# Kernel tuning notes

Hardware: AMD Instinct MI355X
Metric: run time of the kernel (lower is better)

Reference implementation:

```python
import jax, jax.numpy as jnp
import numpy as np

N = 4096
DEG = 16.0
KC = 64  # max closed-neighborhood size supported (deg~16 graph => safe)


def setup_inputs() -> dict:
    key = jax.random.key(0)
    ks = jax.random.split(key, 6)
    u = jax.random.uniform(ks[0], (N, N))
    upper = jnp.triu((u < (DEG / N)).astype(jnp.float32), k=1)
    adj = upper + upper.T  # symmetric 0/1, zero diagonal
    d = 64
    return {
        'adj': adj,
        'e_w': jax.random.normal(ks[1], (15, d), dtype=jnp.float32) * 0.25,
        'e_b': jnp.zeros((d,), jnp.float32),
        'w1': jax.random.normal(ks[2], (3, d, d), dtype=jnp.float32) * 0.125,
        'b1': jnp.zeros((3, d), jnp.float32),
        'w2': jax.random.normal(ks[3], (3, d, d), dtype=jnp.float32) * 0.125,
        'b2': jnp.zeros((3, d), jnp.float32),
        'eps': jnp.zeros((3,), jnp.float32),
    }


def cr_feat(adj):
    n = adj.shape[0]
    m = adj + jnp.eye(n, dtype=adj.dtype)  # closed-neighborhood indicator rows [N,N]
    k = m.sum(1)                            # |S_v|
    D = m @ adj                             # D[v,u] = degree of u inside S_v (A symmetric)
    E = 0.5 * jnp.sum(m * D, axis=1)        # edges inside S_v
    W = jnp.sum(m * D * (D - 1.0) * 0.5, axis=1)  # wedges inside S_v
    vals, idx = jax.lax.top_k(m, KC)        # members of S_v (padded)
    valid = (vals > 0.5).astype(adj.dtype)
    sub = adj[idx[:, :, None], idx[:, None, :]]        # [N,KC,KC] induced subgraph
    sub = sub * valid[:, :, None] * valid[:, None, :]
    T = jnp.einsum('vij,vjk,vki->v', sub, sub, sub) / 6.0  # triangles inside S_v
    f3 = T
    f2 = W - 3.0 * T
    f1 = E * (k - 2.0) - 2.0 * f2 - 3.0 * f3
    tot = k * (k - 1.0) * (k - 2.0) / 6.0   # C(k,3) = total triples
    f0 = tot - f1 - f2 - f3
    f = jnp.stack([f0, f1, f2, f3], axis=1)
    f = jnp.where((k >= 3.0)[:, None], f, 0.0)  # original skips |nb|<3
    return f / (jnp.sum(f, axis=1, keepdims=True) + 1e-10)


def ww_feat(adj):
    a2 = adj @ adj
    a4 = a2 @ a2                             # matrix_power(adj, 4)
    vals, _ = jax.lax.top_k(a4, 8)           # per-row sort desc, top 8
    return vals


def degree_feat(adj):
    d = adj.sum(1)
    diag_a2 = jnp.einsum('vu,uv->v', adj, adj)  # diag(A@A)
    return jnp.stack([d, d ** 2, diag_a2], axis=1)


def _forward(adj, e_w, e_b, w1, b1, w2, b2, eps):
    feats = jnp.concatenate([cr_feat(adj), ww_feat(adj), degree_feat(adj)], axis=1)  # [N,15]
    x = feats @ e_w + e_b
    for i in range(3):
        h = (1.0 + eps[i]) * x + adj @ x
        x = jax.nn.relu(h @ w1[i] + b1[i]) @ w2[i] + b2[i]
    return x.sum(0)


def reference(adj, e_w, e_b, w1, b1, w2, b2, eps):
    return _forward(adj, e_w, e_b, w1, b1, w2, b2, eps)
```

## Files before the change

kernel.cpp:

```cpp
#include <hip/hip_runtime.h>
#include <hip/hip_bf16.h>
#include <stdint.h>

#define NN 4096


__global__ __launch_bounds__(256) void scan_k(const float* __restrict__ adj,
                                              int* __restrict__ nbr,
                                              int* __restrict__ deg,
                                              unsigned long long* __restrict__ abits,
                                              float* __restrict__ feats) {
    __shared__ int nlist[4][64];
    int tid = threadIdx.x;
    int wv = tid >> 6, ln = tid & 63;
    int v = blockIdx.x * 4 + wv;
    size_t rb = (size_t)v * NN;
    int total = 0;
    unsigned long long w0 = 0;
    const float4* row4 = (const float4*)(adj + rb);
    for (int base = 0; base < NN; base += 256) {
        float4 f = row4[(base >> 2) + ln];
        int q4 = (base >> 8) << 2;
        #pragma unroll
        for (int j = 0; j < 4; j++) {
            float vj = (j == 0) ? f.x : (j == 1) ? f.y : (j == 2) ? f.z : f.w;
            unsigned long long m = __ballot(vj > 0.5f);
            if (vj > 0.5f) {
                int pos = total + __popcll(m & ((1ull << ln) - 1ull));
                if (pos < 64) nlist[wv][pos] = base + 4 * ln + j;
            }
            if (ln == q4 + j) w0 = m;
            total += __popcll(m);
        }
    }
    abits[(size_t)v * 64 + ln] = w0;
    int degL = min(total, 64);
    if (ln < degL) nbr[v * 64 + ln] = nlist[wv][ln];
    if (ln == 0) {
        deg[v] = total;
        float degf = (float)total;
        feats[v * 16 + 12] = degf;
        feats[v * 16 + 13] = degf * degf;
        feats[v * 16 + 14] = degf;
    }
}

__global__ __launch_bounds__(256) void cra2_k(const unsigned long long* __restrict__ abits,
                                              const int* __restrict__ nbr,
                                              const int* __restrict__ deg,
                                              unsigned int* __restrict__ a3n,
                                              unsigned int* __restrict__ side,
                                              unsigned int* __restrict__ scnt,
                                              float* __restrict__ feats) {
    __shared__ __align__(64) unsigned int smem[NN + 132 + 640];
    int tid = threadIdx.x;
    int bid = blockIdx.x;
    int wv = tid >> 6, ln = tid & 63;

    if (bid < NN) {
        unsigned int* acc   = smem;
        int* us             = (int*)(smem + NN);
        int* dus            = (int*)(smem + NN + 64);
        unsigned int* wsumS = smem + NN + 128;
        unsigned int* srcL  = smem + NN + 132;
        int v = bid;
        uint4 z = {0u, 0u, 0u, 0u};
        #pragma unroll
        for (int i = 0; i < 4; i++) ((uint4*)acc)[tid + 256 * i] = z;
        int dv = min(deg[v], 64);
        if (tid < dv) {
            int u = nbr[v * 64 + tid];
            us[tid] = u;
            dus[tid] = min(deg[u], 64);
        }
        __syncthreads();
        for (int p = tid; p < dv * 64; p += 256) {
            int i = p >> 6, wi = p & 63;
            if (wi < dus[i]) atomicAdd(&acc[nbr[us[i] * 64 + wi]], 1u);
        }
        __syncthreads();
        unsigned int myw[16];
        int local = 0;
        #pragma unroll
        for (int m = 0; m < 16; m++) {
            unsigned int a = acc[tid + 256 * m];
            myw[m] = a;
            local += (a != 0u);
        }
        int incl = local;
        #pragma unroll
        for (int off = 1; off < 64; off <<= 1) {
            int n = __shfl_up(incl, off, 64);
            if (ln >= off) incl += n;
        }
        if (ln == 63) wsumS[wv] = (unsigned int)incl;
        __syncthreads();
        unsigned int wpre = 0, nsrc = 0;
        #pragma unroll
        for (int q = 0; q < 4; q++) {
            unsigned int s = wsumS[q];
            if (q < wv) wpre += s;
            nsrc += s;
        }
        unsigned int pos = wpre + (unsigned int)(incl - local);
        #pragma unroll
        for (int m = 0; m < 16; m++) {
            unsigned int a = myw[m];
            if (a) {
                unsigned int col = (unsigned int)tid + 256u * m;
                unsigned int dgu = (unsigned int)min(deg[col], 64);
                if (pos < 640u) srcL[pos] = (a << 19) | (dgu << 12) | col;
                pos++;
            }
        }
        if (nsrc > 640u) nsrc = 640u;
        __syncthreads();
        #pragma unroll
        for (int i = 0; i < 4; i++) ((uint4*)acc)[tid + 256 * i] = z;
        __syncthreads();
        int lim64 = (((int)nsrc + 1) >> 1) << 6;
        for (int q = tid; q < lim64; q += 256) {
            int s = ((q >> 6) << 1) | ((q >> 5) & 1);
            int j = q & 31;
            if (s < (int)nsrc) {
                unsigned int e = srcL[s];
                int dgu = (int)((e >> 12) & 0x7Fu);
                unsigned int w = e >> 19;
                const int* nru = nbr + (e & 0xFFFu) * 64;
                if (j < dgu) atomicAdd(&acc[nru[j]], w);
                if (j == 31) {
                    for (int jj = 32; jj < dgu; jj++) atomicAdd(&acc[nru[jj]], w);
                }
            }
        }
        __syncthreads();
        unsigned int wAn = 0, wBn = 0, ovm = 0;
        #pragma unroll
        for (int i2 = 0; i2 < 8; i2++) {
            unsigned int a = acc[16 * tid + i2];
            wAn |= min(a, 15u) << (4 * i2);
            ovm |= (a > 15u ? 1u : 0u) << i2;
        }
        #pragma unroll
        for (int i2 = 0; i2 < 8; i2++) {
            unsigned int a = acc[16 * tid + 8 + i2];
            wBn |= min(a, 15u) << (4 * i2);
            ovm |= (a > 15u ? 1u : 0u) << (8 + i2);
        }
        {
            uint2 nw; nw.x = wAn; nw.y = wBn;
            ((uint2*)(a3n + (size_t)v * 512))[tid] = nw;
        }
        int lov = __popc(ovm);
        int inc2 = lov;
        #pragma unroll
        for (int off = 1; off < 64; off <<= 1) {
            int n = __shfl_up(inc2, off, 64);
            if (ln >= off) inc2 += n;
        }
        if (ln == 63) wsumS[wv] = (unsigned int)inc2;
        __syncthreads();
        unsigned int wpre2 = 0, totS = 0;
        #pragma unroll
        for (int q = 0; q < 4; q++) {
            unsigned int s = wsumS[q];
            if (q < wv) wpre2 += s;
            totS += s;
        }
        unsigned int pos2 = wpre2 + (unsigned int)(inc2 - lov);
        unsigned int* sideR = side + (size_t)v * 192;
        while (ovm) {
            int i2 = __ffs(ovm) - 1;
            ovm &= ovm - 1;
            unsigned int col = (unsigned int)(16 * tid + i2);
            unsigned int a = acc[col];
            if (pos2 < 192u) sideR[pos2] = ((a - 15u) << 16) | col;
            pos2++;
        }
        if (tid == 0) scnt[v] = min(totS, 192u);
    } else {
        unsigned long long* rows = (unsigned long long*)smem;
        int* mems = (int*)(smem + 1024);
        int v = (bid - NN) * 4 + wv;

        int dv = deg[v];
        int degL = min(dv, 64);
        int c = min(dv + 1, 64);

        int nl = (ln < degL) ? nbr[v * 64 + ln] : 0;
        int isless = (ln < degL && nl < v) ? 1 : 0;
        int pos = isless;
        #pragma unroll
        for (int off = 32; off; off >>= 1) pos += __shfl_xor(pos, off, 64);

        int mem = 0;
        if (ln < c) {
            if (ln < pos)       mem = nl;
            else if (ln == pos) mem = v;
            else                mem = nbr[v * 64 + ln - 1];
        }
        mems[wv * 64 + ln] = mem;
        __syncthreads();

        unsigned long long mask = 0ull;
        {
            const unsigned long long* rowb = abits + (size_t)mem * 64;
            for (int j = 0; j < c; j++) {
                int mj = mems[wv * 64 + j];
                unsigned long long w = rowb[((mj >> 8) << 2) | (mj & 3)];
                mask |= ((w >> ((mj >> 2) & 63)) & 1ull) << j;
            }
        }
        if (ln >= c) mask = 0ull;
        rows[wv * 64 + ln] = mask;
        __syncthreads();

        int tpart = 0;
        float epart = 0.f, wpart = 0.f;
        if (ln < c) {
            unsigned long long mm = mask;
            while (mm) {
                int j = __ffsll(mm) - 1;
                mm &= mm - 1;
                tpart += __popcll(mask & rows[wv * 64 + j]);
            }
            if (ln != pos) {
                int cn = __popcll(rows[wv * 64 + pos] & mask);
                float D2 = (float)cn + 1.0f;
                epart = D2;
                wpart = D2 * (D2 - 1.0f) * 0.5f;
            }
        }
        float es = epart, wsum2 = wpart;
        int ts = tpart;
        #pragma unroll
        for (int off = 32; off; off >>= 1) {
            es += __shfl_xor(es, off, 64);
            wsum2 += __shfl_xor(wsum2, off, 64);
            ts += __shfl_xor(ts, off, 64);
        }

        if (ln == 0) {
            float degf = (float)dv;
            float k = degf + 1.0f;
            float E = 0.5f * (es + degf);
            float W = wsum2 + degf * (degf - 1.0f) * 0.5f;
            float T = (float)ts / 6.0f;
            float f3 = T;
            float f2 = W - 3.0f * T;
            float f1 = E * (k - 2.0f) - 2.0f * f2 - 3.0f * f3;
            float tot2 = k * (k - 1.0f) * (k - 2.0f) / 6.0f;
            float f0 = tot2 - f1 - f2 - f3;
            if (k < 3.0f) { f0 = f1 = f2 = f3 = 0.f; }
            float s = f0 + f1 + f2 + f3 + 1e-10f;
            feats[v * 16 + 0] = f0 / s;
            feats[v * 16 + 1] = f1 / s;
            feats[v * 16 + 2] = f2 / s;
            feats[v * 16 + 3] = f3 / s;
        }
    }
}

__global__ __launch_bounds__(1024) void order_k(const int* __restrict__ deg,
                                                int* __restrict__ ord) {
    __shared__ unsigned int bcnt[192];
    __shared__ unsigned int bbase[192];
    int tid = threadIdx.x;
    if (tid < 192) bcnt[tid] = 0u;
    __syncthreads();
    unsigned char myk[4];
    #pragma unroll
    for (int j = 0; j < 4; j++) {
        int v = tid * 4 + j;
        myk[j] = (unsigned char)min(deg[v], 191);
        atomicAdd(&bcnt[myk[j]], 1u);
    }
    __syncthreads();
    if (tid == 0) {
        unsigned int run = 0;
        for (int b = 191; b >= 0; b--) { bbase[b] = run; run += bcnt[b]; }
    }
    __syncthreads();
    #pragma unroll
    for (int j = 0; j < 4; j++) {
        int v = tid * 4 + j;
        unsigned int p = atomicAdd(&bbase[myk[j]], 1u);
        ord[p] = v;
    }
}

__global__ __launch_bounds__(512) void a4row_k(const unsigned int* __restrict__ a3n,
                                               const unsigned int* __restrict__ side,
                                               const unsigned int* __restrict__ scnt,
                                               const int* __restrict__ deg,
                                               const int* __restrict__ nbr,
                                               const int* __restrict__ ord,
                                               const float* __restrict__ feats,
                                               const float* __restrict__ e_w,
                                               const float* __restrict__ e_b,
                                               float* __restrict__ x0) {
    __shared__ unsigned int sacc[NN];
    __shared__ unsigned int sbase[64];
    __shared__ unsigned int sbs[64];
    __shared__ unsigned int sS[64];
    __shared__ unsigned int wtops[64];
    int tid = threadIdx.x;
    int wv = tid >> 6, ln = tid & 63;
    int v = ord[blockIdx.x];

    {
        uint4 z = {0u, 0u, 0u, 0u};
        ((uint4*)sacc)[tid] = z;
        ((uint4*)sacc)[tid + 512] = z;
    }
    int dvv = min(deg[v], 64);
    if (tid < dvv) {
        unsigned int u = (unsigned int)nbr[v * 64 + tid];
        sbase[tid] = u * 512u;
        sbs[tid]   = u * 192u;
        sS[tid]    = scnt[u];
    }
    __syncthreads();

    for (int i = wv; i < dvv; i += 8) {
        int ns = (int)sS[i];
        const unsigned int* sp = side + sbs[i];
        for (int g2 = ln; g2 < ns; g2 += 64) {
            unsigned int e = sp[g2];
            atomicAdd(&sacc[e & 0xFFFu], e >> 16);
        }
    }

    unsigned int aE = 0, aO = 0;
    unsigned int SE0 = 0, SE1 = 0, SO0 = 0, SO1 = 0;
    for (int s0 = 0; s0 < dvv; s0 += 16) {
        int se = min(s0 + 16, dvv);
        for (int s = s0; s < se; s++) {
            unsigned int w = a3n[sbase[s] + (unsigned int)tid];
            aE += w & 0x0F0F0F0Fu;
            aO += (w >> 4) & 0x0F0F0F0Fu;
        }
        SE0 += __builtin_amdgcn_perm(0u, aE, 0x0c010c00u);
        SE1 += __builtin_amdgcn_perm(0u, aE, 0x0c030c02u);
        SO0 += __builtin_amdgcn_perm(0u, aO, 0x0c010c00u);
        SO1 += __builtin_amdgcn_perm(0u, aO, 0x0c030c02u);
        aE = 0; aO = 0;
    }
    __syncthreads();

    uint4 s03 = ((uint4*)sacc)[2 * tid];
    uint4 s47 = ((uint4*)sacc)[2 * tid + 1];
    unsigned int vv[8];
    vv[0] = (SE0 & 0xFFFFu) + s03.x;
    vv[1] = (SO0 & 0xFFFFu) + s03.y;
    vv[2] = (SE0 >> 16)     + s03.z;
    vv[3] = (SO0 >> 16)     + s03.w;
    vv[4] = (SE1 & 0xFFFFu) + s47.x;
    vv[5] = (SO1 & 0xFFFFu) + s47.y;
    vv[6] = (SE1 >> 16)     + s47.z;
    vv[7] = (SO1 >> 16)     + s47.w;

    unsigned int best[8];
    #pragma unroll
    for (int q = 0; q < 8; q++) best[q] = 0u;
    #pragma unroll
    for (int m = 0; m < 8; m++) {
        unsigned int val = vv[m];
        if (val > best[7]) {
            best[7] = val;
            #pragma unroll
            for (int s = 7; s > 0; s--) {
                if (best[s] > best[s - 1]) {
                    unsigned int t2 = best[s - 1]; best[s - 1] = best[s]; best[s] = t2;
                } else break;
            }
        }
    }

    unsigned int wave_val = 0u;
    #pragma unroll
    for (int r = 0; r < 8; r++) {
        unsigned int m = best[0];
        #pragma unroll
        for (int off = 32; off; off >>= 1)
            m = max(m, (unsigned int)__shfl_xor((int)m, off, 64));
        unsigned long long bb = __ballot(best[0] == m);
        int src = __ffsll(bb) - 1;
        if (ln == src) {
            #pragma unroll
            for (int s = 0; s < 7; s++) best[s] = best[s + 1];
            best[7] = 0u;
        }
        if (ln == r) wave_val = m;
    }
    if (ln < 8) wtops[wv * 8 + ln] = wave_val;
    __syncthreads();

    if (wv == 0) {
        unsigned int cand = wtops[ln];
        unsigned int myv = 0u;
        #pragma unroll
        for (int r = 0; r < 8; r++) {
            unsigned int m = cand;
            #pragma unroll
            for (int off = 32; off; off >>= 1)
                m = max(m, (unsigned int)__shfl_xor((int)m, off, 64));
            unsigned long long bb = __ballot(cand == m);
            int src = __ffsll(bb) - 1;
            if (ln == src) cand = 0u;
            if (ln == r) myv = m;
        }
        int d = ln;
        float s = e_b[d];
        s += feats[v * 16 + 0]  * e_w[0 * 64 + d];
        s += feats[v * 16 + 1]  * e_w[1 * 64 + d];
        s += feats[v * 16 + 2]  * e_w[2 * 64 + d];
        s += feats[v * 16 + 3]  * e_w[3 * 64 + d];
        #pragma unroll
        for (int j = 0; j < 8; j++) {
            float mj = (float)(unsigned int)__shfl((int)myv, j, 64);
            s += mj * e_w[(4 + j) * 64 + d];
        }
        s += feats[v * 16 + 12] * e_w[12 * 64 + d];
        s += feats[v * 16 + 13] * e_w[13 * 64 + d];
        s += feats[v * 16 + 14] * e_w[14 * 64 + d];
        x0[(size_t)v * 64 + d] = s;
    }
}

__global__ __launch_bounds__(256) void layer_k(const float* __restrict__ xin,
                                               float* __restrict__ xout,
                                               const float* __restrict__ w1,
                                               const float* __restrict__ b1,
                                               const float* __restrict__ w2,
                                               const float* __restrict__ b2,
                                               const float* __restrict__ eps,
                                               const int* __restrict__ nbr,
                                               const int* __restrict__ deg,
                                               float* __restrict__ out,
                                               int li) {
    __shared__ float wL[4096];
    __shared__ float h[4][64], t[4][64];
    int tid = threadIdx.x;
    int wv = tid >> 6, d = tid & 63;
    int v = blockIdx.x * 4 + wv;

    {
        const float4* src = (const float4*)(w1 + li * 4096);
        #pragma unroll
        for (int i = 0; i < 4; i++) ((float4*)wL)[tid + 256 * i] = src[tid + 256 * i];
    }

    float xv = xin[(size_t)v * 64 + d];
    int dv = min(deg[v], 64);
    const int* nl = nbr + v * 64;
    float agg = 0.f;
    int j = 0;
    for (; j + 4 <= dv; j += 4) {
        int n0 = nl[j], n1 = nl[j + 1], n2 = nl[j + 2], n3 = nl[j + 3];
        float a0 = xin[(size_t)n0 * 64 + d];
        float a1 = xin[(size_t)n1 * 64 + d];
        float a2v = xin[(size_t)n2 * 64 + d];
        float a3 = xin[(size_t)n3 * 64 + d];
        agg += (a0 + a1) + (a2v + a3);
    }
    for (; j < dv; j++) agg += xin[(size_t)nl[j] * 64 + d];
    float hv = (1.0f + eps[li]) * xv + agg;
    h[wv][d] = hv;
    __syncthreads();

    float s = b1[li * 64 + d];
    #pragma unroll 8
    for (int k = 0; k < 64; k++) s += h[wv][k] * wL[k * 64 + d];
    s = fmaxf(s, 0.f);
    t[wv][d] = s;
    __syncthreads();

    {
        const float4* src = (const float4*)(w2 + li * 4096);
        #pragma unroll
        for (int i = 0; i < 4; i++) ((float4*)wL)[tid + 256 * i] = src[tid + 256 * i];
    }
    __syncthreads();

    float o = b2[li * 64 + d];
    #pragma unroll 8
    for (int k = 0; k < 64; k++) o += t[wv][k] * wL[k * 64 + d];
    if (li == 2) {
        h[wv][d] = o;
        __syncthreads();
        if (wv == 0)
            atomicAdd(&out[d], (h[0][d] + h[1][d]) + (h[2][d] + h[3][d]));
    } else {
        xout[(size_t)v * 64 + d] = o;
    }
}

extern "C" void kernel_launch(void* const* d_in, const int* in_sizes, int n_in,
                              void* d_out, int out_size, void* d_ws, size_t ws_size,
                              hipStream_t stream) {
    const float* adj = (const float*)d_in[0];
    const float* e_w = (const float*)d_in[1];
    const float* e_b = (const float*)d_in[2];
    const float* w1  = (const float*)d_in[3];
    const float* b1  = (const float*)d_in[4];
    const float* w2  = (const float*)d_in[5];
    const float* b2  = (const float*)d_in[6];
    const float* eps = (const float*)d_in[7];
    float* out = (float*)d_out;

    char* ws = (char*)d_ws;
    unsigned int*       a3n     = (unsigned int*)(ws);
    unsigned int*       side    = (unsigned int*)(ws + 8388608);
    unsigned int*       scnt    = (unsigned int*)(ws + 11534336);
    int*                nbr     = (int*)(ws + 25165824);
    int*                deg     = (int*)(ws + 26214400);
    float*              feats   = (float*)(ws + 26247168);
    float*              x0      = (float*)(ws + 26509312);
    float*              x1      = (float*)(ws + 27557888);
    unsigned long long* abits   = (unsigned long long*)(ws + 28868608);
    int*                ord     = (int*)(ws + 30969856);

    hipMemsetAsync(out, 0, 64 * sizeof(float), stream);
    scan_k<<<1024, 256, 0, stream>>>(adj, nbr, deg, abits, feats);
    cra2_k<<<5120, 256, 0, stream>>>(abits, nbr, deg, a3n, side, scnt, feats);
    order_k<<<1, 1024, 0, stream>>>(deg, ord);
    a4row_k<<<4096, 512, 0, stream>>>(a3n, side, scnt, deg, nbr, ord, feats, e_w, e_b, x0);
    layer_k<<<1024, 256, 0, stream>>>(x0, x1, w1, b1, w2, b2, eps, nbr, deg, out, 0);
    layer_k<<<1024, 256, 0, stream>>>(x1, x0, w1, b1, w2, b2, eps, nbr, deg, out, 1);
    layer_k<<<1024, 256, 0, stream>>>(x0, x1, w1, b1, w2, b2, eps, nbr, deg, out, 2);
}
```

Before: 259.7 us.

## Flatten neighbor scatter per wave, use DPP max reduction, drop degree ordering

```diff
diff --git a/kernel.cpp b/kernel.cpp
--- a/kernel.cpp
+++ b/kernel.cpp
@@ -4,6 +4,17 @@
 
 #define NN 4096
 
+
+__device__ __forceinline__ unsigned int wave_umax_bcast(unsigned int v) {
+    int x = (int)v;
+    x = max(x, __builtin_amdgcn_update_dpp(0, x, 0x111, 0xF, 0xF, true));
+    x = max(x, __builtin_amdgcn_update_dpp(0, x, 0x112, 0xF, 0xF, true));
+    x = max(x, __builtin_amdgcn_update_dpp(0, x, 0x114, 0xF, 0xF, true));
+    x = max(x, __builtin_amdgcn_update_dpp(0, x, 0x118, 0xF, 0xF, true));
+    x = max(x, __builtin_amdgcn_update_dpp(0, x, 0x142, 0xF, 0xF, true));
+    x = max(x, __builtin_amdgcn_update_dpp(0, x, 0x143, 0xF, 0xF, true));
+    return (unsigned int)__builtin_amdgcn_readlane(x, 63);
+}
 
 __global__ __launch_bounds__(256) void scan_k(const float* __restrict__ adj,
                                               int* __restrict__ nbr,
@@ -52,7 +63,7 @@
                                               unsigned int* __restrict__ side,
                                               unsigned int* __restrict__ scnt,
                                               float* __restrict__ feats) {
-    __shared__ __align__(64) unsigned int smem[NN + 132 + 640];
+    __shared__ __align__(64) unsigned int smem[NN + 132 + 648];
     int tid = threadIdx.x;
     int bid = blockIdx.x;
     int wv = tid >> 6, ln = tid & 63;
@@ -117,20 +128,33 @@
         __syncthreads();
         #pragma unroll
         for (int i = 0; i < 4; i++) ((uint4*)acc)[tid + 256 * i] = z;
-        __syncthreads();
-        int lim64 = (((int)nsrc + 1) >> 1) << 6;
-        for (int q = tid; q < lim64; q += 256) {
-            int s = ((q >> 6) << 1) | ((q >> 5) & 1);
-            int j = q & 31;
-            if (s < (int)nsrc) {
-                unsigned int e = srcL[s];
-                int dgu = (int)((e >> 12) & 0x7Fu);
-                unsigned int w = e >> 19;
-                const int* nru = nbr + (e & 0xFFFu) * 64;
-                if (j < dgu) atomicAdd(&acc[nru[j]], w);
-                if (j == 31) {
-                    for (int jj = 32; jj < dgu; jj++) atomicAdd(&acc[nru[jj]], w);
-                }
+        int nsrc8 = (((int)nsrc + 7) >> 3) << 3;
+        if (tid < nsrc8 - (int)nsrc) srcL[(int)nsrc + tid] = 0u;
+        __syncthreads();
+        for (int i0 = wv * 8; i0 < nsrc8; i0 += 32) {
+            uint4 qa = *(const uint4*)&srcL[i0];
+            uint4 qb = *(const uint4*)&srcL[i0 + 4];
+            int c1 = (int)((qa.x >> 12) & 0x7Fu);
+            int c2 = c1 + (int)((qa.y >> 12) & 0x7Fu);
+            int c3 = c2 + (int)((qa.z >> 12) & 0x7Fu);
+            int c4 = c3 + (int)((qa.w >> 12) & 0x7Fu);
+            int c5 = c4 + (int)((qb.x >> 12) & 0x7Fu);
+            int c6 = c5 + (int)((qb.y >> 12) & 0x7Fu);
+            int c7 = c6 + (int)((qb.z >> 12) & 0x7Fu);
+            int tot = c7 + (int)((qb.w >> 12) & 0x7Fu);
+            unsigned int s0 = ((qa.x & 0xFFFu) * 64u)                                | (qa.x & 0xFFF80000u);
+            unsigned int s1 = ((((qa.y & 0xFFFu) * 64u) - (unsigned int)c1) & 0x7FFFFu) | (qa.y & 0xFFF80000u);
+            unsigned int s2 = ((((qa.z & 0xFFFu) * 64u) - (unsigned int)c2) & 0x7FFFFu) | (qa.z & 0xFFF80000u);
+            unsigned int s3 = ((((qa.w & 0xFFFu) * 64u) - (unsigned int)c3) & 0x7FFFFu) | (qa.w & 0xFFF80000u);
+            unsigned int s4 = ((((qb.x & 0xFFFu) * 64u) - (unsigned int)c4) & 0x7FFFFu) | (qb.x & 0xFFF80000u);
+            unsigned int s5 = ((((qb.y & 0xFFFu) * 64u) - (unsigned int)c5) & 0x7FFFFu) | (qb.y & 0xFFF80000u);
+            unsigned int s6 = ((((qb.z & 0xFFFu) * 64u) - (unsigned int)c6) & 0x7FFFFu) | (qb.z & 0xFFF80000u);
+            unsigned int s7 = ((((qb.w & 0xFFFu) * 64u) - (unsigned int)c7) & 0x7FFFFu) | (qb.w & 0xFFF80000u);
+            for (int g = ln; g < tot; g += 64) {
+                unsigned int sel = (g < c1) ? s0 : (g < c2) ? s1 : (g < c3) ? s2 : (g < c4) ? s3
+                                 : (g < c5) ? s4 : (g < c6) ? s5 : (g < c7) ? s6 : s7;
+                unsigned int idx = (sel + (unsigned int)g) & 0x7FFFFu;
+                atomicAdd(&acc[nbr[idx]], sel >> 19);
             }
         }
         __syncthreads();
@@ -261,40 +285,11 @@
     }
 }
 
-__global__ __launch_bounds__(1024) void order_k(const int* __restrict__ deg,
-                                                int* __restrict__ ord) {
-    __shared__ unsigned int bcnt[192];
-    __shared__ unsigned int bbase[192];
-    int tid = threadIdx.x;
-    if (tid < 192) bcnt[tid] = 0u;
-    __syncthreads();
-    unsigned char myk[4];
-    #pragma unroll
-    for (int j = 0; j < 4; j++) {
-        int v = tid * 4 + j;
-        myk[j] = (unsigned char)min(deg[v], 191);
-        atomicAdd(&bcnt[myk[j]], 1u);
-    }
-    __syncthreads();
-    if (tid == 0) {
-        unsigned int run = 0;
-        for (int b = 191; b >= 0; b--) { bbase[b] = run; run += bcnt[b]; }
-    }
-    __syncthreads();
-    #pragma unroll
-    for (int j = 0; j < 4; j++) {
-        int v = tid * 4 + j;
-        unsigned int p = atomicAdd(&bbase[myk[j]], 1u);
-        ord[p] = v;
-    }
-}
-
 __global__ __launch_bounds__(512) void a4row_k(const unsigned int* __restrict__ a3n,
                                                const unsigned int* __restrict__ side,
                                                const unsigned int* __restrict__ scnt,
                                                const int* __restrict__ deg,
                                                const int* __restrict__ nbr,
-                                               const int* __restrict__ ord,
                                                const float* __restrict__ feats,
                                                const float* __restrict__ e_w,
                                                const float* __restrict__ e_b,
@@ -306,7 +301,7 @@
     __shared__ unsigned int wtops[64];
     int tid = threadIdx.x;
     int wv = tid >> 6, ln = tid & 63;
-    int v = ord[blockIdx.x];
+    int v = blockIdx.x;
 
     {
         uint4 z = {0u, 0u, 0u, 0u};
@@ -380,10 +375,7 @@
     unsigned int wave_val = 0u;
     #pragma unroll
     for (int r = 0; r < 8; r++) {
-        unsigned int m = best[0];
-        #pragma unroll
-        for (int off = 32; off; off >>= 1)
-            m = max(m, (unsigned int)__shfl_xor((int)m, off, 64));
+        unsigned int m = wave_umax_bcast(best[0]);
         unsigned long long bb = __ballot(best[0] == m);
         int src = __ffsll(bb) - 1;
         if (ln == src) {
@@ -401,10 +393,7 @@
         unsigned int myv = 0u;
         #pragma unroll
         for (int r = 0; r < 8; r++) {
-            unsigned int m = cand;
-            #pragma unroll
-            for (int off = 32; off; off >>= 1)
-                m = max(m, (unsigned int)__shfl_xor((int)m, off, 64));
+            unsigned int m = wave_umax_bcast(cand);
             unsigned long long bb = __ballot(cand == m);
             int src = __ffsll(bb) - 1;
             if (ln == src) cand = 0u;
@@ -519,13 +508,11 @@
     float*              x0      = (float*)(ws + 26509312);
     float*              x1      = (float*)(ws + 27557888);
     unsigned long long* abits   = (unsigned long long*)(ws + 28868608);
-    int*                ord     = (int*)(ws + 30969856);
 
     hipMemsetAsync(out, 0, 64 * sizeof(float), stream);
     scan_k<<<1024, 256, 0, stream>>>(adj, nbr, deg, abits, feats);
     cra2_k<<<5120, 256, 0, stream>>>(abits, nbr, deg, a3n, side, scnt, feats);
-    order_k<<<1, 1024, 0, stream>>>(deg, ord);
-    a4row_k<<<4096, 512, 0, stream>>>(a3n, side, scnt, deg, nbr, ord, feats, e_w, e_b, x0);
+    a4row_k<<<4096, 512, 0, stream>>>(a3n, side, scnt, deg, nbr, feats, e_w, e_b, x0);
     layer_k<<<1024, 256, 0, stream>>>(x0, x1, w1, b1, w2, b2, eps, nbr, deg, out, 0);
     layer_k<<<1024, 256, 0, stream>>>(x1, x0, w1, b1, w2, b2, eps, nbr, deg, out, 1);
     layer_k<<<1024, 256, 0, stream>>>(x0, x1, w1, b1, w2, b2, eps, nbr, deg, out, 2);
```

Result: no change. 255.7 us (-1.5%).
